# Performance work log

Hardware: AMD Instinct MI355X
Metric: run time of the kernel (lower is better)

Reference implementation:

```python
import jax, jax.numpy as jnp
import numpy as np

H = 128          # hidden_channels
N_USER = 100000
N_ITEM = 50000
E = 1000000      # number of labeled edges


def setup_inputs() -> dict:
    key = jax.random.key(0)
    ks = jax.random.split(key, 6)
    z_user = jax.random.normal(ks[0], (N_USER, H), dtype=jnp.float32)
    z_item = jax.random.normal(ks[1], (N_ITEM, H), dtype=jnp.float32)
    row = jax.random.randint(ks[2], (E,), 0, N_USER, dtype=jnp.int64 if jax.config.jax_enable_x64 else jnp.int32)
    col = jax.random.randint(ks[3], (E,), 0, N_ITEM, dtype=jnp.int64 if jax.config.jax_enable_x64 else jnp.int32)
    W1 = jax.random.normal(ks[4], (2 * H, H), dtype=jnp.float32) / np.sqrt(2 * H)
    b1 = jnp.zeros((H,), dtype=jnp.float32)
    W2 = jax.random.normal(ks[5], (H, 1), dtype=jnp.float32) / np.sqrt(H)
    b2 = jnp.zeros((1,), dtype=jnp.float32)
    return {"z_user": z_user, "z_item": z_item, "row": row, "col": col,
            "W1": W1, "b1": b1, "W2": W2, "b2": b2}


def reference(z_user, z_item, row, col, W1, b1, W2, b2):
    # z = cat([z_user[row], z_item[col]], -1); lin1(z).relu(); lin2 -> view(-1)
    # Split W1 so we never materialize the [E, 2H] concat explicitly as one buffer:
    # cat([a, b]) @ W1 == a @ W1[:H] + b @ W1[H:]
    W1u, W1i = W1[:H], W1[H:]
    h = z_user[row] @ W1u + z_item[col] @ W1i + b1          # [E, H]
    h = jax.nn.relu(h)
    out = h @ W2 + b2                                        # [E, 1]
    return out.reshape(-1)
```

## Files before the change

### kernel.cpp

```cpp
#include <hip/hip_runtime.h>

#define HH 128
#define BU 8
#define BI 32
#define NBKT (BU * BI)
#define SCHUNK 2048

typedef __attribute__((ext_vector_type(8))) short bf16x8;
typedef __attribute__((ext_vector_type(4))) float f32x4;
typedef _Float16 h2 __attribute__((ext_vector_type(2)));

#if __has_builtin(__builtin_amdgcn_fdot2)
#define FDOT2(a, b, c) __builtin_amdgcn_fdot2((a), (b), (c), false)
#else
#define FDOT2(a, b, c) ((c) + (float)(a)[0] * (float)(b)[0] + (float)(a)[1] * (float)(b)[1])
#endif

__device__ inline unsigned short f2bf(float f) {
    unsigned u = __builtin_bit_cast(unsigned, f);
    u += 0x7FFF + ((u >> 16) & 1);
    return (unsigned short)(u >> 16);
}
__device__ inline unsigned short f2h(float f) {
    return __builtin_bit_cast(unsigned short, (_Float16)f);
}

__global__ __launch_bounds__(256) void scatter_kernel(
    const int* __restrict__ row, const int* __restrict__ col,
    unsigned* __restrict__ cursor, unsigned* __restrict__ srt,
    unsigned* __restrict__ invpos, int E, unsigned n_user, unsigned n_item, int cap)
{
    __shared__ unsigned lh[NBKT];
    __shared__ unsigned gb[NBKT];
    __shared__ unsigned lc[NBKT];
    const int t    = threadIdx.x;
    const int base = blockIdx.x * SCHUNK;

    int uu[SCHUNK / 256], ii[SCHUNK / 256];
    lh[t] = 0;
    __syncthreads();
    #pragma unroll
    for (int k = 0; k < SCHUNK / 256; ++k) {
        int e = base + k * 256 + t;
        if (e < E) {
            uu[k] = row[e]; ii[k] = col[e];
            unsigned uc = ((unsigned)uu[k] * BU) / n_user;
            unsigned ic = ((unsigned)ii[k] * BI) / n_item;
            atomicAdd(&lh[uc * BI + ic], 1u);
        }
    }
    __syncthreads();
    gb[t] = lh[t] ? (unsigned)(t * cap) + atomicAdd(&cursor[t], lh[t]) : 0u;
    lc[t] = 0;
    __syncthreads();
    #pragma unroll
    for (int k = 0; k < SCHUNK / 256; ++k) {
        int e = base + k * 256 + t;
        if (e < E) {
            unsigned uc = ((unsigned)uu[k] * BU) / n_user;
            unsigned ic = ((unsigned)ii[k] * BI) / n_item;
            int b = (int)(uc * BI + ic);
            unsigned ucbase = (uc * n_user + 7u) >> 3;
            unsigned r   = atomicAdd(&lc[b], 1u);
            unsigned pos = gb[b] + r;
            srt[pos]  = (((unsigned)uu[k] - ucbase) << 16) | (unsigned)ii[k];
            invpos[e] = pos;
        }
    }
}

__global__ __launch_bounds__(256) void project_both_kernel(
    const float* __restrict__ Zu, const float* __restrict__ Zi,
    const float* __restrict__ W1, const float* __restrict__ b1,
    unsigned short* __restrict__ Pu, unsigned short* __restrict__ Pi,
    int n_user, int n_item, int ublocks)
{
    __shared__ unsigned short sWt[128 * 128];
    __shared__ unsigned short sOut[64 * 136];

    const bool isUser = ((int)blockIdx.x < ublocks);
    const float* __restrict__ Z = isUser ? Zu : Zi;
    const float* __restrict__ W = isUser ? W1 : (W1 + HH * HH);
    unsigned short* __restrict__ P = isUser ? Pu : Pi;
    const int nrows  = isUser ? n_user : n_item;
    const int ntiles = (nrows + 63) >> 6;
    const int tbase  = (isUser ? (int)blockIdx.x : ((int)blockIdx.x - ublocks)) * 2;

    const int t    = threadIdx.x;
    const int wave = t >> 6;
    const int lane = t & 63;
    const int l16  = lane & 15;
    const int lk8  = (lane >> 4) * 8;

    #pragma unroll 4
    for (int i = 0; i < 16; ++i) {
        int idx = t + i * 256;
        int k   = idx >> 5;
        int c4  = (idx & 31) * 4;
        float4 w = *(const float4*)(W + (size_t)k * HH + c4);
        float wv[4] = {w.x, w.y, w.z, w.w};
        #pragma unroll
        for (int j = 0; j < 4; ++j) {
            int c = c4 + j;
            sWt[c * 128 + (((k >> 3) ^ (c & 15)) << 3) + (k & 7)] = f2bf(wv[j]);
        }
    }

    float b1r[8];
    #pragma unroll
    for (int nt = 0; nt < 8; ++nt)
        b1r[nt] = isUser ? b1[nt * 16 + l16] : 0.f;

    __syncthreads();

    #pragma unroll 1
    for (int s = 0; s < 2; ++s) {
        const int tile = tbase + s;
        if (tile >= ntiles) break;
        const int rbase = tile << 6;

        f32x4 acc[8];
        #pragma unroll
        for (int nt = 0; nt < 8; ++nt) acc[nt] = (f32x4)0.f;

        int m = rbase + wave * 16 + l16;
        if (m > nrows - 1) m = nrows - 1;
        const float* Zrow = Z + (size_t)m * HH;

        #pragma unroll
        for (int kk = 0; kk < 4; ++kk) {
            float4 z0 = *(const float4*)(Zrow + kk * 32 + lk8);
            float4 z1 = *(const float4*)(Zrow + kk * 32 + lk8 + 4);
            bf16x8 a;
            a[0] = (short)f2bf(z0.x); a[1] = (short)f2bf(z0.y);
            a[2] = (short)f2bf(z0.z); a[3] = (short)f2bf(z0.w);
            a[4] = (short)f2bf(z1.x); a[5] = (short)f2bf(z1.y);
            a[6] = (short)f2bf(z1.z); a[7] = (short)f2bf(z1.w);

            const int chunkSw = ((kk * 4 + (lane >> 4)) ^ l16) << 3;
            #pragma unroll
            for (int nt = 0; nt < 8; ++nt) {
                int c = nt * 16 + l16;
                bf16x8 b = *(const bf16x8*)(sWt + c * 128 + chunkSw);
                acc[nt] = __builtin_amdgcn_mfma_f32_16x16x32_bf16(a, b, acc[nt], 0, 0, 0);
            }
        }

        __syncthreads();
        #pragma unroll
        for (int nt = 0; nt < 8; ++nt) {
            int colc = nt * 16 + l16;
            #pragma unroll
            for (int r = 0; r < 4; ++r) {
                int orow = wave * 16 + (lane >> 4) * 4 + r;
                sOut[orow * 136 + colc] = f2h(acc[nt][r] + b1r[nt]);
            }
        }
        __syncthreads();
        #pragma unroll
        for (int i = 0; i < 4; ++i) {
            int idx = t + i * 256;
            int r   = idx >> 4;
            int ch  = idx & 15;
            int grow = rbase + r;
            if (grow < nrows)
                *(uint4*)(P + (size_t)grow * HH + ch * 8) =
                    *(const uint4*)(sOut + r * 136 + ch * 8);
        }
    }
}

__global__ __launch_bounds__(256) void edge_sorted_kernel(
    const unsigned short* __restrict__ Pu, const unsigned short* __restrict__ Pi,
    const unsigned* __restrict__ srt, const unsigned* __restrict__ cursor,
    const float* __restrict__ W2, const float* __restrict__ b2,
    float* __restrict__ psorted, int cap, int n_user)
{
    const int uc     = blockIdx.x & (BU - 1);
    const int jj     = blockIdx.x >> 3;
    const int g      = threadIdx.x >> 3;
    const int lane8  = threadIdx.x & 7;
    const int gg     = jj * 32 + g;
    const int c0     = lane8 * 16;
    const int ucbase = (int)(((unsigned)uc * (unsigned)n_user + 7u) >> 3);

    h2 w2h[8];
    #pragma unroll
    for (int j = 0; j < 8; ++j) {
        w2h[j][0] = (_Float16)W2[c0 + 2 * j];
        w2h[j][1] = (_Float16)W2[c0 + 2 * j + 1];
    }
    const float b2s = b2[0];
    const h2 hz = {(_Float16)0, (_Float16)0};

    #pragma unroll 1
    for (int ic = 0; ic < BI; ++ic) {
        const int b    = uc * BI + ic;
        const int S    = b * cap;
        const int Tend = S + (int)cursor[b];
        for (int p = S + gg; p < Tend; p += BU * 1024) {
            unsigned pk = srt[p];
            int u  = ucbase + (int)(pk >> 16);
            int it = (int)(pk & 0xFFFFu);
            const unsigned short* pur = Pu + (size_t)u  * HH + c0;
            const unsigned short* pir = Pi + (size_t)it * HH + c0;
            uint4 a0 = *(const uint4*)pur;
            uint4 a1 = *(const uint4*)(pur + 8);
            uint4 c0v = *(const uint4*)pir;
            uint4 c1v = *(const uint4*)(pir + 8);
            unsigned aw[8] = {a0.x, a0.y, a0.z, a0.w, a1.x, a1.y, a1.z, a1.w};
            unsigned cw[8] = {c0v.x, c0v.y, c0v.z, c0v.w, c1v.x, c1v.y, c1v.z, c1v.w};
            float acc = 0.f;
            #pragma unroll
            for (int q = 0; q < 8; ++q) {
                h2 s = __builtin_bit_cast(h2, aw[q]) + __builtin_bit_cast(h2, cw[q]);
                s = __builtin_elementwise_max(s, hz);
                acc = FDOT2(s, w2h[q], acc);
            }
            acc += __shfl_xor(acc, 4, 64);
            acc += __shfl_xor(acc, 2, 64);
            acc += __shfl_xor(acc, 1, 64);
            if (lane8 == 0) psorted[p] = acc + b2s;
        }
    }
}

__global__ __launch_bounds__(256) void permute_kernel(
    const float* __restrict__ psorted, const unsigned* __restrict__ invpos,
    float* __restrict__ out, int E)
{
    int i  = blockIdx.x * blockDim.x + threadIdx.x;
    int st = gridDim.x * blockDim.x;
    for (int e = i; e < E; e += st)
        out[e] = psorted[invpos[e]];
}

__global__ __launch_bounds__(256) void edge_fp16_kernel(
    const unsigned short* __restrict__ Pu, const unsigned short* __restrict__ Pi,
    const int* __restrict__ row, const int* __restrict__ col,
    const float* __restrict__ W2, const float* __restrict__ b2,
    float* __restrict__ out, int E)
{
    const int lane8  = threadIdx.x & 7;
    const int gid    = (blockIdx.x * blockDim.x + threadIdx.x) >> 3;
    const int stride = (gridDim.x * blockDim.x) >> 3;
    const int c0     = lane8 * 16;

    h2 w2h[8];
    #pragma unroll
    for (int j = 0; j < 8; ++j) {
        w2h[j][0] = (_Float16)W2[c0 + 2 * j];
        w2h[j][1] = (_Float16)W2[c0 + 2 * j + 1];
    }
    const float b2s = b2[0];
    const h2 hz = {(_Float16)0, (_Float16)0};

    for (int e = gid; e < E; e += stride) {
        int u = row[e], it = col[e];
        const unsigned short* pur = Pu + (size_t)u  * HH + c0;
        const unsigned short* pir = Pi + (size_t)it * HH + c0;
        uint4 a0 = *(const uint4*)pur;
        uint4 a1 = *(const uint4*)(pur + 8);
        uint4 c0v = *(const uint4*)pir;
        uint4 c1v = *(const uint4*)(pir + 8);
        unsigned aw[8] = {a0.x, a0.y, a0.z, a0.w, a1.x, a1.y, a1.z, a1.w};
        unsigned cw[8] = {c0v.x, c0v.y, c0v.z, c0v.w, c1v.x, c1v.y, c1v.z, c1v.w};
        float acc = 0.f;
        #pragma unroll
        for (int q = 0; q < 8; ++q) {
            h2 s = __builtin_bit_cast(h2, aw[q]) + __builtin_bit_cast(h2, cw[q]);
            s = __builtin_elementwise_max(s, hz);
            acc = FDOT2(s, w2h[q], acc);
        }
        acc += __shfl_xor(acc, 4, 64);
        acc += __shfl_xor(acc, 2, 64);
        acc += __shfl_xor(acc, 1, 64);
        if (lane8 == 0) out[e] = acc + b2s;
    }
}

__global__ __launch_bounds__(256) void edge_direct_kernel(
    const float* __restrict__ zu, const float* __restrict__ zi,
    const int* __restrict__ row, const int* __restrict__ col,
    const float* __restrict__ W1, const float* __restrict__ b1,
    const float* __restrict__ W2, const float* __restrict__ b2,
    float* __restrict__ out, int E)
{
    const int lane   = threadIdx.x & 31;
    const int gid    = (blockIdx.x * blockDim.x + threadIdx.x) >> 5;
    const int stride = (gridDim.x * blockDim.x) >> 5;
    const int c0     = lane * 4;

    const float4 b1v = *(const float4*)(b1 + c0);
    const float4 w2v = *(const float4*)(W2 + c0);
    const float  b2s = b2[0];

    for (int e = gid; e < E; e += stride) {
        int u  = row[e];
        int it = col[e];
        const float* zur = zu + (size_t)u  * HH;
        const float* zir = zi + (size_t)it * HH;
        float4 acc = b1v;
        for (int k = 0; k < HH; ++k) {
            float  zk = zur[k];
            float4 w  = *(const float4*)(W1 + (size_t)k * HH + c0);
            acc.x = fmaf(zk, w.x, acc.x);
            acc.y = fmaf(zk, w.y, acc.y);
            acc.z = fmaf(zk, w.z, acc.z);
            acc.w = fmaf(zk, w.w, acc.w);
        }
        for (int k = 0; k < HH; ++k) {
            float  zk = zir[k];
            float4 w  = *(const float4*)(W1 + (size_t)(HH + k) * HH + c0);
            acc.x = fmaf(zk, w.x, acc.x);
            acc.y = fmaf(zk, w.y, acc.y);
            acc.z = fmaf(zk, w.z, acc.z);
            acc.w = fmaf(zk, w.w, acc.w);
        }
        float p = fmaxf(acc.x, 0.f) * w2v.x;
        p = fmaf(fmaxf(acc.y, 0.f), w2v.y, p);
        p = fmaf(fmaxf(acc.z, 0.f), w2v.z, p);
        p = fmaf(fmaxf(acc.w, 0.f), w2v.w, p);
        #pragma unroll
        for (int m = 16; m >= 1; m >>= 1)
            p += __shfl_xor(p, m, 64);
        if (lane == 0) out[e] = p + b2s;
    }
}

static inline size_t align256(size_t x) { return (x + 255) & ~(size_t)255; }

extern "C" void kernel_launch(void* const* d_in, const int* in_sizes, int n_in,
                              void* d_out, int out_size, void* d_ws, size_t ws_size,
                              hipStream_t stream)
{
    const float* z_user = (const float*)d_in[0];
    const float* z_item = (const float*)d_in[1];
    const int*   row    = (const int*)d_in[2];
    const int*   col    = (const int*)d_in[3];
    const float* W1     = (const float*)d_in[4];
    const float* b1     = (const float*)d_in[5];
    const float* W2     = (const float*)d_in[6];
    const float* b2     = (const float*)d_in[7];
    float*       out    = (float*)d_out;

    const int n_user = in_sizes[0] / HH;
    const int n_item = in_sizes[1] / HH;
    const int E      = in_sizes[2];

    const int capBase = (E + NBKT - 1) / NBKT;
    const int cap     = capBase + capBase / 4 + 64;
    const size_t padded = (size_t)cap * NBKT;

    const size_t offPu  = 0;
    const size_t offPi  = align256(offPu  + (size_t)n_user * HH * 2);
    const size_t offSrt = align256(offPi  + (size_t)n_item * HH * 2);
    const size_t offPs  = align256(offSrt + padded * 4);
    const size_t offInv = align256(offPs  + padded * 4);
    const size_t offCur = align256(offInv + (size_t)E * 4);
    const size_t needSort = align256(offCur + NBKT * 4);
    const size_t needProj = align256(offPi + (size_t)n_item * HH * 2);

    const bool sortable = (n_user >= BU) && (n_item >= BI) &&
                          (n_item < 65536) && (n_user / BU + 1 < 65536) &&
                          (n_user <= (1 << 17)) && (ws_size >= needSort);

    const int utiles  = (n_user + 63) >> 6;
    const int itiles  = (n_item + 63) >> 6;
    const int ublocks = (utiles + 1) >> 1;
    const int iblocks = (itiles + 1) >> 1;
    const int scatBlocks = (E + SCHUNK - 1) / SCHUNK;

    if (sortable) {
        unsigned short* Pu  = (unsigned short*)((char*)d_ws + offPu);
        unsigned short* Pi  = (unsigned short*)((char*)d_ws + offPi);
        unsigned*       srt = (unsigned*)((char*)d_ws + offSrt);
        float*          ps  = (float*)((char*)d_ws + offPs);
        unsigned*       inv = (unsigned*)((char*)d_ws + offInv);
        unsigned*       cur = (unsigned*)((char*)d_ws + offCur);

        hipMemsetAsync(cur, 0, NBKT * 4, stream);
        scatter_kernel<<<scatBlocks, 256, 0, stream>>>(
            row, col, cur, srt, inv, E, (unsigned)n_user, (unsigned)n_item, cap);
        project_both_kernel<<<ublocks + iblocks, 256, 0, stream>>>(
            z_user, z_item, W1, b1, Pu, Pi, n_user, n_item, ublocks);
        edge_sorted_kernel<<<2048, 256, 0, stream>>>(Pu, Pi, srt, cur, W2, b2, ps, cap, n_user);
        permute_kernel<<<1024, 256, 0, stream>>>(ps, inv, out, E);
    } else if (ws_size >= needProj) {
        unsigned short* Pu = (unsigned short*)((char*)d_ws + offPu);
        unsigned short* Pi = (unsigned short*)((char*)d_ws + offPi);
        project_both_kernel<<<ublocks + iblocks, 256, 0, stream>>>(
            z_user, z_item, W1, b1, Pu, Pi, n_user, n_item, ublocks);
        edge_fp16_kernel<<<2048, 256, 0, stream>>>(Pu, Pi, row, col, W2, b2, out, E);
    } else {
        edge_direct_kernel<<<2048, 256, 0, stream>>>(z_user, z_item, row, col, W1, b1, W2, b2, out, E);
    }
}
```

Baseline: 108.8 us.

## Pretranspose W1 once and make projection kernel persistent; halve item buckets

Adds a small kernel that converts W1 to a swizzled bf16 transposed layout once, so each projection block only copies it into LDS instead of converting it per block. The projection kernel becomes a grid-stride persistent kernel capped at 768 blocks and restages weights only when switching between user and item halves. The item bucket count drops from 32 to 16, which changes sort locality and edge-kernel striding. This adds one extra launch, and the lower bucket count may reduce cache locality of item rows.

```diff
diff --git a/kernel.cpp b/kernel.cpp
--- a/kernel.cpp
+++ b/kernel.cpp
@@ -2,9 +2,10 @@
 
 #define HH 128
 #define BU 8
-#define BI 32
+#define BI 16
 #define NBKT (BU * BI)
 #define SCHUNK 2048
+#define GPUC 8192
 
 typedef __attribute__((ext_vector_type(8))) short bf16x8;
 typedef __attribute__((ext_vector_type(4))) float f32x4;
@@ -25,6 +26,26 @@
     return __builtin_bit_cast(unsigned short, (_Float16)f);
 }
 
+__global__ __launch_bounds__(256) void wt_kernel(
+    const float* __restrict__ W1, unsigned short* __restrict__ Wt)
+{
+    const int gid = blockIdx.x * 256 + threadIdx.x;
+    const int h   = gid >> 11;
+    const int c   = (gid >> 4) & 127;
+    const int kc  = gid & 15;
+    const float* src = W1 + (size_t)(h * 128 + kc * 8) * HH + c;
+    unsigned short v[8];
+    #pragma unroll
+    for (int d = 0; d < 8; ++d)
+        v[d] = f2bf(src[(size_t)d * HH]);
+    uint4 pack;
+    pack.x = (unsigned)v[0] | ((unsigned)v[1] << 16);
+    pack.y = (unsigned)v[2] | ((unsigned)v[3] << 16);
+    pack.z = (unsigned)v[4] | ((unsigned)v[5] << 16);
+    pack.w = (unsigned)v[6] | ((unsigned)v[7] << 16);
+    *(uint4*)(Wt + (size_t)h * 16384 + c * 128 + ((kc ^ (c & 15)) << 3)) = pack;
+}
+
 __global__ __launch_bounds__(256) void scatter_kernel(
     const int* __restrict__ row, const int* __restrict__ col,
     unsigned* __restrict__ cursor, unsigned* __restrict__ srt,
@@ -37,7 +58,7 @@
     const int base = blockIdx.x * SCHUNK;
 
     int uu[SCHUNK / 256], ii[SCHUNK / 256];
-    lh[t] = 0;
+    if (t < NBKT) lh[t] = 0;
     __syncthreads();
     #pragma unroll
     for (int k = 0; k < SCHUNK / 256; ++k) {
@@ -50,8 +71,10 @@
         }
     }
     __syncthreads();
-    gb[t] = lh[t] ? (unsigned)(t * cap) + atomicAdd(&cursor[t], lh[t]) : 0u;
-    lc[t] = 0;
+    if (t < NBKT) {
+        gb[t] = lh[t] ? (unsigned)(t * cap) + atomicAdd(&cursor[t], lh[t]) : 0u;
+        lc[t] = 0;
+    }
     __syncthreads();
     #pragma unroll
     for (int k = 0; k < SCHUNK / 256; ++k) {
@@ -69,55 +92,48 @@
     }
 }
 
-__global__ __launch_bounds__(256) void project_both_kernel(
+__global__ __launch_bounds__(256) void project_kernel(
     const float* __restrict__ Zu, const float* __restrict__ Zi,
-    const float* __restrict__ W1, const float* __restrict__ b1,
+    const unsigned short* __restrict__ Wt, const float* __restrict__ b1,
     unsigned short* __restrict__ Pu, unsigned short* __restrict__ Pi,
-    int n_user, int n_item, int ublocks)
+    int n_user, int n_item, int utiles, int itiles)
 {
     __shared__ unsigned short sWt[128 * 128];
     __shared__ unsigned short sOut[64 * 136];
-
-    const bool isUser = ((int)blockIdx.x < ublocks);
-    const float* __restrict__ Z = isUser ? Zu : Zi;
-    const float* __restrict__ W = isUser ? W1 : (W1 + HH * HH);
-    unsigned short* __restrict__ P = isUser ? Pu : Pi;
-    const int nrows  = isUser ? n_user : n_item;
-    const int ntiles = (nrows + 63) >> 6;
-    const int tbase  = (isUser ? (int)blockIdx.x : ((int)blockIdx.x - ublocks)) * 2;
 
     const int t    = threadIdx.x;
     const int wave = t >> 6;
     const int lane = t & 63;
     const int l16  = lane & 15;
     const int lk8  = (lane >> 4) * 8;
-
-    #pragma unroll 4
-    for (int i = 0; i < 16; ++i) {
-        int idx = t + i * 256;
-        int k   = idx >> 5;
-        int c4  = (idx & 31) * 4;
-        float4 w = *(const float4*)(W + (size_t)k * HH + c4);
-        float wv[4] = {w.x, w.y, w.z, w.w};
-        #pragma unroll
-        for (int j = 0; j < 4; ++j) {
-            int c = c4 + j;
-            sWt[c * 128 + (((k >> 3) ^ (c & 15)) << 3) + (k & 7)] = f2bf(wv[j]);
-        }
-    }
-
-    float b1r[8];
-    #pragma unroll
-    for (int nt = 0; nt < 8; ++nt)
-        b1r[nt] = isUser ? b1[nt * 16 + l16] : 0.f;
-
-    __syncthreads();
-
-    #pragma unroll 1
-    for (int s = 0; s < 2; ++s) {
-        const int tile = tbase + s;
-        if (tile >= ntiles) break;
-        const int rbase = tile << 6;
+    const int total = utiles + itiles;
+
+    int staged = -1;
+
+    for (int tid = blockIdx.x; tid < total; tid += gridDim.x) {
+        const bool isUser = (tid < utiles);
+        const int  half   = isUser ? 0 : 1;
+        const float* __restrict__ Z = isUser ? Zu : Zi;
+        unsigned short* __restrict__ P = isUser ? Pu : Pi;
+        const int nrows = isUser ? n_user : n_item;
+        const int rbase = (isUser ? tid : (tid - utiles)) << 6;
+
+        if (half != staged) {
+            __syncthreads();
+            const unsigned short* src = Wt + (size_t)half * 16384;
+            #pragma unroll
+            for (int i = 0; i < 16; ++i) {
+                int off = (i * 256 + t) * 8;
+                *(uint4*)(sWt + off) = *(const uint4*)(src + off);
+            }
+            __syncthreads();
+            staged = half;
+        }
+
+        float b1r[8];
+        #pragma unroll
+        for (int nt = 0; nt < 8; ++nt)
+            b1r[nt] = isUser ? b1[nt * 16 + l16] : 0.f;
 
         f32x4 acc[8];
         #pragma unroll
@@ -198,7 +214,7 @@
         const int b    = uc * BI + ic;
         const int S    = b * cap;
         const int Tend = S + (int)cursor[b];
-        for (int p = S + gg; p < Tend; p += BU * 1024) {
+        for (int p = S + gg; p < Tend; p += GPUC) {
             unsigned pk = srt[p];
             int u  = ucbase + (int)(pk >> 16);
             int it = (int)(pk & 0xFFFFu);
@@ -352,7 +368,8 @@
     const int cap     = capBase + capBase / 4 + 64;
     const size_t padded = (size_t)cap * NBKT;
 
-    const size_t offPu  = 0;
+    const size_t offWt  = 0;
+    const size_t offPu  = align256(offWt  + 32768 * 2);
     const size_t offPi  = align256(offPu  + (size_t)n_user * HH * 2);
     const size_t offSrt = align256(offPi  + (size_t)n_item * HH * 2);
     const size_t offPs  = align256(offSrt + padded * 4);
@@ -365,13 +382,14 @@
                           (n_item < 65536) && (n_user / BU + 1 < 65536) &&
                           (n_user <= (1 << 17)) && (ws_size >= needSort);
 
-    const int utiles  = (n_user + 63) >> 6;
-    const int itiles  = (n_item + 63) >> 6;
-    const int ublocks = (utiles + 1) >> 1;
-    const int iblocks = (itiles + 1) >> 1;
+    const int utiles = (n_user + 63) >> 6;
+    const int itiles = (n_item + 63) >> 6;
+    const int total  = utiles + itiles;
+    const int pgrid  = total < 768 ? total : 768;
     const int scatBlocks = (E + SCHUNK - 1) / SCHUNK;
 
     if (sortable) {
+        unsigned short* Wt  = (unsigned short*)((char*)d_ws + offWt);
         unsigned short* Pu  = (unsigned short*)((char*)d_ws + offPu);
         unsigned short* Pi  = (unsigned short*)((char*)d_ws + offPi);
         unsigned*       srt = (unsigned*)((char*)d_ws + offSrt);
@@ -380,17 +398,20 @@
         unsigned*       cur = (unsigned*)((char*)d_ws + offCur);
 
         hipMemsetAsync(cur, 0, NBKT * 4, stream);
+        wt_kernel<<<16, 256, 0, stream>>>(W1, Wt);
         scatter_kernel<<<scatBlocks, 256, 0, stream>>>(
             row, col, cur, srt, inv, E, (unsigned)n_user, (unsigned)n_item, cap);
-        project_both_kernel<<<ublocks + iblocks, 256, 0, stream>>>(
-            z_user, z_item, W1, b1, Pu, Pi, n_user, n_item, ublocks);
+        project_kernel<<<pgrid, 256, 0, stream>>>(
+            z_user, z_item, Wt, b1, Pu, Pi, n_user, n_item, utiles, itiles);
         edge_sorted_kernel<<<2048, 256, 0, stream>>>(Pu, Pi, srt, cur, W2, b2, ps, cap, n_user);
         permute_kernel<<<1024, 256, 0, stream>>>(ps, inv, out, E);
     } else if (ws_size >= needProj) {
+        unsigned short* Wt = (unsigned short*)((char*)d_ws + offWt);
         unsigned short* Pu = (unsigned short*)((char*)d_ws + offPu);
         unsigned short* Pi = (unsigned short*)((char*)d_ws + offPi);
-        project_both_kernel<<<ublocks + iblocks, 256, 0, stream>>>(
-            z_user, z_item, W1, b1, Pu, Pi, n_user, n_item, ublocks);
+        wt_kernel<<<16, 256, 0, stream>>>(W1, Wt);
+        project_kernel<<<pgrid, 256, 0, stream>>>(
+            z_user, z_item, Wt, b1, Pu, Pi, n_user, n_item, utiles, itiles);
         edge_fp16_kernel<<<2048, 256, 0, stream>>>(Pu, Pi, row, col, W2, b2, out, E);
     } else {
         edge_direct_kernel<<<2048, 256, 0, stream>>>(z_user, z_item, row, col, W1, b1, W2, b2, out, E);
```

New measurement: 100.8 us. -7.3%, faster.
